# Performance work log

Hardware: AMD Instinct MI355X
Metric: run time of the kernel (lower is better)

## Reference

```python
import jax, jax.numpy as jnp
import numpy as np

# irreps as (multiplicity, l); parities match between in/hidden/out so every irrep has exactly one path
IRR_IN  = [(256, 0), (128, 1), (64, 2)]   # dim 256+384+320 = 960
IRR_H   = [(512, 0), (256, 1), (128, 2)]  # dim 512+768+640 = 1920
IRR_OUT = IRR_IN
N = 32768
EPS = 1e-8      # NormActivation epsilon
BN_EPS = 1e-5   # BatchNorm eps (e3nn default)


def _dim(irr):
    return sum(m * (2 * l + 1) for m, l in irr)


def _split(x, irr):
    """Split flat [N, dim] into per-irrep fields [N, mul, 2l+1]."""
    outs, o = [], 0
    for m, l in irr:
        d = m * (2 * l + 1)
        outs.append(x[:, o:o + d].reshape(x.shape[0], m, 2 * l + 1))
        o += d
    return outs


def _linear(x, w, irr_in, irr_out):
    """e3nn o3.Linear: per-irrep channel mixing with 1/sqrt(fan_in) path norm, no bias."""
    fields = _split(x, irr_in)
    outs, o = [], 0
    for f, (mi, l), (mo, _) in zip(fields, irr_in, irr_out):
        wk = w[o:o + mi * mo].reshape(mi, mo) * (1.0 / np.sqrt(mi))
        o += mi * mo
        outs.append(jnp.einsum('nui,uv->nvi', f, wk).reshape(f.shape[0], -1))
    return jnp.concatenate(outs, axis=1)


def _norm_act(x, irr):
    """e3nn NormActivation(scalar_nonlinearity=sigmoid, normalize=True): f * sigmoid(|f|)/|f|."""
    outs = []
    for f in _split(x, irr):
        n = jnp.sqrt(jnp.sum(f * f, axis=-1, keepdims=True) + EPS)
        outs.append((f * (jax.nn.sigmoid(n) / n)).reshape(f.shape[0], -1))
    return jnp.concatenate(outs, axis=1)


def _batch_norm(x, w, b, irr):
    """e3nn BatchNorm (training mode, reduce='mean', normalization='component').
    Scalars: standard batchnorm with weight+bias. l>0: divide by sqrt(batch-mean
    component-squared-norm), scale by weight."""
    outs, ow, ob = [], 0, 0
    for f, (m, l) in zip(_split(x, irr), irr):
        wk = w[ow:ow + m]; ow += m
        if l == 0:
            bk = b[ob:ob + m]; ob += m
            mu = jnp.mean(f, axis=0)                      # [m, 1]
            var = jnp.mean((f - mu) ** 2, axis=0)         # [m, 1]
            g = (f - mu) * (wk[:, None] / jnp.sqrt(var + BN_EPS)) + bk[:, None]
        else:
            n2 = jnp.mean(jnp.mean(f * f, axis=-1), axis=0)  # [m]
            g = f * (wk / jnp.sqrt(n2 + BN_EPS))[None, :, None]
        outs.append(g.reshape(f.shape[0], -1))
    return jnp.concatenate(outs, axis=1)


def setup_inputs() -> dict:
    key = jax.random.key(0)
    ks = jax.random.split(key, 5)
    n_w1 = sum(mi * mo for (mi, _), (mo, _) in zip(IRR_IN, IRR_H))    # 172032
    n_w2 = sum(mi * mo for (mi, _), (mo, _) in zip(IRR_H, IRR_H))     # 344064
    n_w3 = sum(mi * mo for (mi, _), (mo, _) in zip(IRR_H, IRR_OUT))   # 172032
    n_wb = sum(mi * mo for (mi, _), (mo, _) in zip(IRR_IN, IRR_OUT))  # 86016
    return {
        'x': jax.random.normal(ks[0], (N, _dim(IRR_IN)), dtype=jnp.float32),
        'w1': jax.random.normal(ks[1], (n_w1,), dtype=jnp.float32),
        'w2': jax.random.normal(ks[2], (n_w2,), dtype=jnp.float32),
        'w3': jax.random.normal(ks[3], (n_w3,), dtype=jnp.float32),
        'wb': jax.random.normal(ks[4], (n_wb,), dtype=jnp.float32),
        'bn_w': jnp.ones((448,), dtype=jnp.float32),
        'bn_b': jnp.zeros((256,), dtype=jnp.float32),
    }


def reference(x, w1, w2, w3, wb, bn_w, bn_b):
    out = _linear(x, w1, IRR_IN, IRR_H)
    out = _norm_act(out, IRR_H)
    out = _linear(out, w2, IRR_H, IRR_H)
    out = _norm_act(out, IRR_H)
    out = _linear(out, w3, IRR_H, IRR_OUT)
    out = _linear(x, wb, IRR_IN, IRR_OUT) + out
    return _batch_norm(out, bn_w, bn_b, IRR_OUT)
```

## Files before the change

### kernel.cpp

```cpp
#include <hip/hip_runtime.h>
#include <cstddef>
#include <cstdint>

#define DEVINL __device__ __forceinline__
typedef unsigned short u16;
typedef __attribute__((ext_vector_type(8))) short short8;
typedef __attribute__((ext_vector_type(4))) float f32x4;
#define MFMA16 __builtin_amdgcn_mfma_f32_16x16x32_bf16

constexpr int NROW = 32768;
constexpr int CM   = 8192;

constexpr size_t WT_B    = 0;
constexpr size_t STATS_B = 3014656;
constexpr size_t XS0_B   = 3017728;
constexpr size_t X1_B    = 53349376;
constexpr size_t X2_B    = 103681024;
constexpr size_t H1S0_B  = 145624064;
constexpr size_t H1S1_B  = 162401280;
constexpr size_t H1S2_B  = 187567104;
constexpr size_t Y0F_B   = 145624064;
constexpr size_t Y1_B    = 179178496;
constexpr size_t Y2_B    = 204344320;
constexpr size_t WS_NEED = 225315840;


DEVINL u16 f2bf(float f) { union { float f; unsigned u; } c; c.f = f;
    unsigned r = (c.u + 0x7fffu + ((c.u >> 16) & 1u)) >> 16; return (u16)r; }
DEVINL float bf2f(u16 b) { union { unsigned u; float f; } c; c.u = ((unsigned)b) << 16; return c.f; }
DEVINL short8 ld8(const u16* p) { return *(const short8*)p; }

DEVINL void gload16(const u16* g, u16* l) {
    __builtin_amdgcn_global_load_lds(
        (const __attribute__((address_space(1))) unsigned*)g,
        (__attribute__((address_space(3))) unsigned*)l, 16, 0, 0);
}

__global__ void k_prep(const float* __restrict__ w1, const float* __restrict__ w2,
                       const float* __restrict__ w3, const float* __restrict__ wb,
                       u16* __restrict__ WT, float* __restrict__ stats)
{
    int t = blockIdx.x * 256 + threadIdx.x;
    if (t < 1507328) {
        const float iA = 0.08838834764831845f;
        const float iB = 0.044194173824159216f;
        const int   beg[12]  = {0,393216,458752,475136,999424,1130496,1163264,1294336,1327104,1335296,1466368,1499136};
        const int   rowW[12] = {768,256,128,1024,512,256,512,256,128,512,256,128};
        const int   l2K[12]  = {8,7,6,9,8,7,9,8,7,8,7,6};
        const int   srco[12] = {0,131072,163840,0,262144,327680,0,131072,163840,0,65536,81920};
        const int   arr[12]  = {0,0,0,1,1,1,2,2,2,3,3,3};
        const int   ld[12]   = {512,256,128,512,256,128,256,128,64,256,128,64};
        const float scl[12]  = {0.0625f,iA,0.125f,iB,0.0625f,iA,iB,0.0625f,iA,0.0625f,iA,0.125f};
        int s = 0;
        #pragma unroll
        for (int i = 1; i < 12; ++i) s += (t >= beg[i]) ? 1 : 0;
        int e    = t - beg[s];
        int v    = e / rowW[s];
        int rem  = e - v * rowW[s];
        int limb = rem >> l2K[s];
        int u    = rem & ((1 << l2K[s]) - 1);
        const float* srcs[4] = {w1, w2, w3, wb};
        float val = srcs[arr[s]][srco[s] + u * ld[s] + v] * scl[s];
        u16 h = f2bf(val);  float r1 = val - bf2f(h);
        u16 m = f2bf(r1);   float r2 = r1 - bf2f(m);
        WT[t] = (limb == 0) ? h : (limb == 1) ? m : f2bf(r2);
    } else {
        int q = t - 1507328;
        if (q < 704) stats[q] = 0.f;
    }
}

__global__ void k_xconv(const float* __restrict__ x, u16* __restrict__ xs0,
                        u16* __restrict__ x1, u16* __restrict__ x2)
{
    int g = blockIdx.x * 256 + threadIdx.x;
    if (g < 1048576) {
        int n = g >> 5, u0 = (g & 31) * 8;
        const float* s = x + (size_t)n * 960 + u0;
        float4 f0 = *(const float4*)s;
        float4 f1 = *(const float4*)(s + 4);
        float f[8] = {f0.x,f0.y,f0.z,f0.w,f1.x,f1.y,f1.z,f1.w};
        short8 oh, om, ol;
        #pragma unroll
        for (int j = 0; j < 8; ++j) {
            u16 h = f2bf(f[j]); float r1 = f[j] - bf2f(h);
            u16 m = f2bf(r1);   float r2 = r1 - bf2f(m);
            oh[j] = (short)h; om[j] = (short)m; ol[j] = (short)f2bf(r2);
        }
        size_t d = (size_t)n * 768 + u0;
        *(short8*)(xs0 + d) = oh;
        *(short8*)(xs0 + d + 256) = om;
        *(short8*)(xs0 + d + 512) = ol;
        return;
    }
    float f[8]; u16* dst; int halfW;
    if (g < 2621440) {
        int gl = g - 1048576;
        int i = gl >> 19, r = gl & 524287;
        int n = r >> 4, u0 = (r & 15) * 8;
        const float* s = x + (size_t)n * 960 + 256 + (size_t)u0 * 3 + i;
        #pragma unroll
        for (int j = 0; j < 8; ++j) f[j] = s[j * 3];
        dst = x1 + (size_t)i * 8388608 + (size_t)n * 256 + u0;
        halfW = 128;
    } else {
        int gl = g - 2621440;
        int i = gl >> 18, r = gl & 262143;
        int n = r >> 3, u0 = (r & 7) * 8;
        const float* s = x + (size_t)n * 960 + 640 + (size_t)u0 * 5 + i;
        #pragma unroll
        for (int j = 0; j < 8; ++j) f[j] = s[j * 5];
        dst = x2 + (size_t)i * 4194304 + (size_t)n * 128 + u0;
        halfW = 64;
    }
    short8 oh, ol;
    #pragma unroll
    for (int j = 0; j < 8; ++j) {
        u16 h = f2bf(f[j]);
        oh[j] = (short)h;
        ol[j] = (short)f2bf(f[j] - bf2f(h));
    }
    *(short8*)dst = oh;
    *(short8*)(dst + halfW) = ol;
}

template<int NT, int EP, bool TS, bool SEG2>
__global__ __launch_bounds__(256) void k_gemm(
    const u16* __restrict__ A1, long A1ps, int A1cmb, int A1rs,
    int K1, int k1t, int T1, unsigned a1map, unsigned b1map,
    const u16* __restrict__ B1, int B1rs,
    const u16* __restrict__ A2, long A2ps, int A2cmb, int A2rs,
    int K2, int k2t, unsigned a2map, unsigned b2map,
    const u16* __restrict__ B2, int B2rs,
    int Stot, int tsTiles,
    u16* __restrict__ outB, float* __restrict__ outF,
    long Ops, int Ocmb, int Ors, int loOff, int cbs)
{
    constexpr int BN = NT * 32;
    __shared__ u16 lds[2][128 * 64];

    int b = blockIdx.x;
    int xcd = b & 7, jj = b >> 3;
    int rb = xcd + ((jj >> cbs) << 3);
    int cb = jj & ((1 << cbs) - 1);
    int rb128 = rb << 7;

    int tix = threadIdx.x, lane = tix & 63, w = tix >> 6;
    int wm64 = (w >> 1) << 6;
    int wn = w & 1;

    const u16* a1row = A1 + (size_t)(rb128 >> A1cmb) * A1ps
                          + (size_t)(rb128 & ((1 << A1cmb) - 1)) * A1rs;
    const u16* a2row = nullptr;
    if constexpr (SEG2)
        a2row = A2 + (size_t)(rb128 >> A2cmb) * A2ps
                   + (size_t)(rb128 & ((1 << A2cmb) - 1)) * A2rs;

    auto stage = [&](int t, int buf) {
        const u16* art; int rs, col0;
        if (!SEG2 || t < T1) {
            int sg = t >> k1t, off = (t & ((1 << k1t) - 1)) << 6;
            art = a1row; rs = A1rs;
            col0 = (int)((a1map >> (2 * sg)) & 3u) * K1 + off;
        } else {
            int tt = t - T1;
            int sg = tt >> k2t, off = (tt & ((1 << k2t) - 1)) << 6;
            art = a2row; rs = A2rs;
            col0 = (int)((a2map >> (2 * sg)) & 3u) * K2 + off;
        }
        #pragma unroll
        for (int i = 0; i < 4; ++i) {
            int seg = (w << 2) | i;
            int tr  = (seg << 3) + (lane >> 3);
            int sl  = lane & 7;
            const u16* src = art + (size_t)tr * rs + col0 + ((sl ^ (tr & 7)) << 3);
            gload16(src, &lds[buf][seg * 512]);
        }
    };

    f32x4 z = {0.f, 0.f, 0.f, 0.f};
    f32x4 acc[4][NT], S[4][NT], E[4][NT];
    #pragma unroll
    for (int mt = 0; mt < 4; ++mt)
        #pragma unroll
        for (int nt = 0; nt < NT; ++nt) { acc[mt][nt] = z; if constexpr (TS) { S[mt][nt] = z; E[mt][nt] = z; } }

    stage(0, 0);
    asm volatile("s_waitcnt vmcnt(0)" ::: "memory");
    __syncthreads();

    int colbase = cb * BN + wn * (NT * 16) + (lane & 15);
    int cur = 0;
    for (int s = 0; s < Stot; ++s) {
        const u16* bp; int brs, bcol;
        if (!SEG2 || s < T1) {
            int sg = s >> k1t;
            bcol = (int)((b1map >> (2 * sg)) & 3u) * K1 + ((s & ((1 << k1t) - 1)) << 6);
            bp = B1; brs = B1rs;
        } else {
            int tt = s - T1; int sg = tt >> k2t;
            bcol = (int)((b2map >> (2 * sg)) & 3u) * K2 + ((tt & ((1 << k2t) - 1)) << 6);
            bp = B2; brs = B2rs;
        }
        short8 breg[NT][2];
        #pragma unroll
        for (int nt = 0; nt < NT; ++nt)
            #pragma unroll
            for (int h = 0; h < 2; ++h)
                breg[nt][h] = ld8(bp + (size_t)(colbase + nt * 16) * brs + bcol + h * 32 + ((lane >> 4) << 3));

        if (s + 1 < Stot) stage(s + 1, cur ^ 1);

        bool tsT = TS && (s < tsTiles);
        #pragma unroll
        for (int h = 0; h < 2; ++h) {
            short8 a[4];
            #pragma unroll
            for (int mt = 0; mt < 4; ++mt) {
                int tr = wm64 + mt * 16 + (lane & 15);
                int slot = h * 4 + (lane >> 4);
                a[mt] = *(const short8*)&lds[cur][tr * 64 + ((slot ^ (tr & 7)) << 3)];
            }
            if (tsT) {
                #pragma unroll
                for (int mt = 0; mt < 4; ++mt)
                    #pragma unroll
                    for (int nt = 0; nt < NT; ++nt) {
                        f32x4 d = MFMA16(a[mt], breg[nt][h], z, 0, 0, 0);
                        #pragma unroll
                        for (int r = 0; r < 4; ++r) {
                            float aa = S[mt][nt][r], bb = d[r];
                            float sm = aa + bb;
                            float tt2 = sm - aa;
                            float er = (aa - (sm - tt2)) + (bb - tt2);
                            S[mt][nt][r] = sm;
                            E[mt][nt][r] += er;
                        }
                    }
            } else {
                #pragma unroll
                for (int mt = 0; mt < 4; ++mt)
                    #pragma unroll
                    for (int nt = 0; nt < NT; ++nt)
                        acc[mt][nt] = MFMA16(a[mt], breg[nt][h], acc[mt][nt], 0, 0, 0);
            }
        }
        asm volatile("s_waitcnt vmcnt(0)" ::: "memory");
        __syncthreads();
        cur ^= 1;
    }

    size_t obase = (size_t)(rb128 >> Ocmb) * Ops + (size_t)(rb128 & ((1 << Ocmb) - 1)) * Ors;
    #pragma unroll
    for (int mt = 0; mt < 4; ++mt) {
        #pragma unroll
        for (int r = 0; r < 4; ++r) {
            int lrow = wm64 + mt * 16 + ((lane >> 4) << 2) + r;
            size_t ro = obase + (size_t)lrow * Ors;
            #pragma unroll
            for (int nt = 0; nt < NT; ++nt) {
                int colg = cb * BN + wn * (NT * 16) + nt * 16 + (lane & 15);
                float p = acc[mt][nt][r];
                if constexpr (TS) p = S[mt][nt][r] + (E[mt][nt][r] + p);
                if constexpr (EP == 1) {
                    outF[ro + colg] = p;
                } else {
                    float v = p;
                    if constexpr (EP == 2 || EP == 3) {
                        float nrm = sqrtf(p * p + 1e-8f);
                        v = p / ((1.0f + expf(-nrm)) * nrm);
                    }
                    u16 hi = f2bf(v);
                    outB[ro + colg] = hi;
                    if constexpr (EP == 3 || EP == 4)
                        outB[ro + colg + loOff] = f2bf(v - bf2f(hi));
                }
            }
        }
    }
}

template<int C, bool SPL>
__global__ __launch_bounds__(256) void k_normact(u16* __restrict__ buf, long PS,
                                                 int l2g, int halfW, long total8)
{
    long idx = (long)blockIdx.x * 256 + threadIdx.x;
    if (idx >= total8) return;
    long r  = idx >> l2g;
    int  cg = (int)(idx & ((1 << l2g) - 1));
    int  W  = SPL ? (halfW << 1) : halfW;
    size_t off = (size_t)r * W + (size_t)cg * 8;
    float f[C][8];
    #pragma unroll
    for (int i = 0; i < C; ++i) {
        short8 h = ld8(buf + (size_t)i * PS + off);
        if constexpr (SPL) {
            short8 l = ld8(buf + (size_t)i * PS + off + halfW);
            #pragma unroll
            for (int j = 0; j < 8; ++j) f[i][j] = bf2f((u16)h[j]) + bf2f((u16)l[j]);
        } else {
            #pragma unroll
            for (int j = 0; j < 8; ++j) f[i][j] = bf2f((u16)h[j]);
        }
    }
    #pragma unroll
    for (int j = 0; j < 8; ++j) {
        float s2 = 1e-8f;
        #pragma unroll
        for (int i = 0; i < C; ++i) s2 += f[i][j] * f[i][j];
        float nrm = sqrtf(s2);
        float scl = 1.0f / ((1.0f + __expf(-nrm)) * nrm);
        #pragma unroll
        for (int i = 0; i < C; ++i) f[i][j] *= scl;
    }
    #pragma unroll
    for (int i = 0; i < C; ++i) {
        short8 oh, ol;
        #pragma unroll
        for (int j = 0; j < 8; ++j) {
            u16 hi = f2bf(f[i][j]);
            oh[j] = (short)hi;
            if constexpr (SPL) ol[j] = (short)f2bf(f[i][j] - bf2f(hi));
        }
        *(short8*)(buf + (size_t)i * PS + off) = oh;
        if constexpr (SPL) *(short8*)(buf + (size_t)i * PS + off + halfW) = ol;
    }
}

__global__ void k_stats(const float* __restrict__ y0f, const u16* __restrict__ y1,
                        const u16* __restrict__ y2, float* __restrict__ stats)
{
    int sec = blockIdx.y, t = threadIdx.x;
    int r0 = blockIdx.x * 512;
    float sm = 0.f, sq = 0.f;
    if (sec == 0) {
        int v = t;
        for (int r = r0; r < r0 + 512; ++r) {
            float val = y0f[(size_t)r * 256 + v];
            sm += val; sq += val * val;
        }
        atomicAdd(&stats[v], sm);
        atomicAdd(&stats[256 + v], sq);
    } else if (sec == 1) {
        int v = t & 127, sub = t >> 7;
        for (int r = r0 + sub; r < r0 + 512; r += 2)
            #pragma unroll
            for (int p = 0; p < 3; ++p) {
                float val = bf2f(y1[(size_t)p * 4194304 + (size_t)r * 128 + v]);
                sq += val * val;
            }
        __shared__ float S2[256];
        S2[t] = sq; __syncthreads();
        if (t < 128) atomicAdd(&stats[512 + v], sq + S2[t + 128]);
    } else {
        int v = t & 63, sub = t >> 6;
        for (int r = r0 + sub; r < r0 + 512; r += 4)
            #pragma unroll
            for (int p = 0; p < 5; ++p) {
                float val = bf2f(y2[(size_t)p * 2097152 + (size_t)r * 64 + v]);
                sq += val * val;
            }
        __shared__ float S2[256];
        S2[t] = sq; __syncthreads();
        if (t < 64) atomicAdd(&stats[640 + v], sq + S2[t + 64] + S2[t + 128] + S2[t + 192]);
    }
}

__global__ __launch_bounds__(448) void k_bnapply(
    const float* __restrict__ y0f, const u16* __restrict__ y1, const u16* __restrict__ y2,
    const float* __restrict__ stats, const float* __restrict__ bnw, const float* __restrict__ bnb,
    float* __restrict__ out)
{
    int n = blockIdx.x, t = threadIdx.x;
    const float invN = 1.f / 32768.f;
    if (t < 256) {
        float mu  = stats[t] * invN;
        float var = stats[256 + t] * invN - mu * mu;
        float a   = bnw[t] * rsqrtf(var + 1e-5f);
        out[(size_t)n * 960 + t] = (y0f[(size_t)n * 256 + t] - mu) * a + bnb[t];
    } else if (t < 384) {
        int v = t - 256;
        float a = bnw[256 + v] * rsqrtf(stats[512 + v] * (invN / 3.f) + 1e-5f);
        #pragma unroll
        for (int i = 0; i < 3; ++i)
            out[(size_t)n * 960 + 256 + v * 3 + i] =
                bf2f(y1[(size_t)i * 4194304 + (size_t)n * 128 + v]) * a;
    } else {
        int v = t - 384;
        float a = bnw[384 + v] * rsqrtf(stats[640 + v] * (invN / 5.f) + 1e-5f);
        #pragma unroll
        for (int i = 0; i < 5; ++i)
            out[(size_t)n * 960 + 640 + v * 5 + i] =
                bf2f(y2[(size_t)i * 2097152 + (size_t)n * 64 + v]) * a;
    }
}

extern "C" void kernel_launch(void* const* d_in, const int* in_sizes, int n_in,
                              void* d_out, int out_size, void* d_ws, size_t ws_size,
                              hipStream_t stream)
{
    const float* x   = (const float*)d_in[0];
    const float* w1  = (const float*)d_in[1];
    const float* w2  = (const float*)d_in[2];
    const float* w3  = (const float*)d_in[3];
    const float* wb  = (const float*)d_in[4];
    const float* bnw = (const float*)d_in[5];
    const float* bnb = (const float*)d_in[6];
    float* out = (float*)d_out;

    if (ws_size < WS_NEED) return;

    char* ws = (char*)d_ws;
    u16*   WT    = (u16*)(ws + WT_B);
    float* stats = (float*)(ws + STATS_B);
    u16*   xs0   = (u16*)(ws + XS0_B);
    u16*   x1    = (u16*)(ws + X1_B);
    u16*   x2    = (u16*)(ws + X2_B);
    u16*   h1s0  = (u16*)(ws + H1S0_B);
    u16*   h1s1  = (u16*)(ws + H1S1_B);
    u16*   h1s2  = (u16*)(ws + H1S2_B);
    float* y0f   = (float*)(ws + Y0F_B);
    u16*   y1    = (u16*)(ws + Y1_B);
    u16*   y2    = (u16*)(ws + Y2_B);
    u16*   h2s0  = (u16*)d_out;
    u16*   h2s1  = h2s0 + 16777216;
    u16*   h2s2  = h2s0 + 41943040;

    k_prep <<<5891, 256, 0, stream>>>(w1, w2, w3, wb, WT, stats);
    k_xconv<<<15360, 256, 0, stream>>>(x, xs0, x1, x2);

    for (int c = 0; c < NROW / CM; ++c) {
        size_t r0 = (size_t)c * CM;
        k_gemm<2, 3, true, false><<<512, 256, 0, stream>>>(
            xs0 + r0 * 768, 0L, 30, 768,
            256, 2, 24, 580u, 2128u, WT + 0, 768,
            nullptr, 0L, 30, 64, 64, 0, 0u, 0u, nullptr, 64,
            24, 4,
            h1s0, nullptr, 0L, 30, 1024, 512, 3);
        k_gemm<4, 4, false, false><<<384, 256, 0, stream>>>(
            x1 + r0 * 256, 8388608L, 13, 256,
            128, 1, 6, 4u, 16u, WT + 393216, 256,
            nullptr, 0L, 30, 64, 64, 0, 0u, 0u, nullptr, 64,
            6, 0,
            h1s1, nullptr, 4194304L, 13, 512, 256, 1);
        k_gemm<4, 4, false, false><<<320, 256, 0, stream>>>(
            x2 + r0 * 128, 4194304L, 13, 128,
            64, 0, 3, 4u, 16u, WT + 458752, 128,
            nullptr, 0L, 30, 64, 64, 0, 0u, 0u, nullptr, 64,
            3, 0,
            h1s2, nullptr, 2097152L, 13, 256, 128, 0);
        k_normact<3, true><<<1024, 256, 0, stream>>>(h1s1, 4194304L, 5, 256, 262144L);
        k_normact<5, true><<<512,  256, 0, stream>>>(h1s2, 2097152L, 4, 128, 131072L);
        k_gemm<4, 2, false, false><<<256, 256, 0, stream>>>(
            h1s0, 0L, 30, 1024,
            512, 3, 24, 4u, 16u, WT + 475136, 1024,
            nullptr, 0L, 30, 64, 64, 0, 0u, 0u, nullptr, 64,
            24, 0,
            h2s0 + r0 * 512, nullptr, 0L, 30, 512, 0, 2);
        k_gemm<4, 0, false, false><<<384, 256, 0, stream>>>(
            h1s1, 4194304L, 13, 512,
            256, 2, 12, 4u, 16u, WT + 999424, 512,
            nullptr, 0L, 30, 64, 64, 0, 0u, 0u, nullptr, 64,
            12, 0,
            h2s1 + r0 * 256, nullptr, 8388608L, 13, 256, 0, 1);
        k_gemm<4, 0, false, false><<<320, 256, 0, stream>>>(
            h1s2, 2097152L, 13, 256,
            128, 1, 6, 4u, 16u, WT + 1130496, 256,
            nullptr, 0L, 30, 64, 64, 0, 0u, 0u, nullptr, 64,
            6, 0,
            h2s2 + r0 * 128, nullptr, 4194304L, 13, 128, 0, 0);
    }
    k_normact<3, false><<<4096, 256, 0, stream>>>(h2s1, 8388608L, 5, 256, 1048576L);
    k_normact<5, false><<<2048, 256, 0, stream>>>(h2s2, 4194304L, 4, 128, 524288L);

    k_gemm<4, 1, false, true><<<512, 256, 0, stream>>>(
        h2s0, 0L, 30, 512,
        512, 3, 8, 0u, 0u, WT + 1163264, 512,
        xs0, 0L, 30, 768,
        256, 2, 4u, 16u, WT + 1335296, 512,
        20, 0,
        nullptr, y0f, 0L, 30, 256, 0, 1);
    k_gemm<4, 0, false, true><<<768, 256, 0, stream>>>(
        h2s1, 8388608L, 15, 256,
        256, 2, 4, 0u, 0u, WT + 1294336, 256,
        x1, 8388608L, 15, 256,
        128, 1, 4u, 16u, WT + 1466368, 256,
        10, 0,
        y1, nullptr, 4194304L, 15, 128, 0, 0);
    k_gemm<2, 0, false, true><<<1280, 256, 0, stream>>>(
        h2s2, 4194304L, 15, 128,
        128, 1, 2, 0u, 0u, WT + 1327104, 128,
        x2, 4194304L, 15, 128,
        64, 0, 4u, 16u, WT + 1499136, 128,
        5, 0,
        y2, nullptr, 2097152L, 15, 64, 0, 0);

    k_stats  <<<dim3(64, 3), 256, 0, stream>>>(y0f, y1, y2, stats);
    k_bnapply<<<32768, 448, 0, stream>>>(y0f, y1, y2, stats, bnw, bnb, out);
}
```

Baseline: 1.363 ms.

## Merge per-irrep GEMMs into grouped launches with triple-buffered LDS pipeline

Groups the three per-irrep GEMMs of each layer into one launch that dispatches on block index through a descriptor struct. It also fuses the two norm-activation kernels and rewrites input conversion to stage rows in LDS for coalesced reads. The GEMM main loop moves from double to triple buffering with partial vmcnt waits, so two tiles are in flight and barriers are lighter. Block-to-tile mapping drops the XCD-aware swizzle, and stats uses more blocks. The aim is fewer launches, less tail idle time and better load/compute overlap, at the cost of extra LDS per block (lower occupancy) and possibly worse L2 locality.

```diff
diff --git a/kernel.cpp b/kernel.cpp
--- a/kernel.cpp
+++ b/kernel.cpp
@@ -23,7 +23,6 @@
 constexpr size_t Y1_B    = 179178496;
 constexpr size_t Y2_B    = 204344320;
 constexpr size_t WS_NEED = 225315840;
-
 
 DEVINL u16 f2bf(float f) { union { float f; unsigned u; } c; c.f = f;
     unsigned r = (c.u + 0x7fffu + ((c.u >> 16) & 1u)) >> 16; return (u16)r; }
@@ -70,111 +69,109 @@
     }
 }
 
-__global__ void k_xconv(const float* __restrict__ x, u16* __restrict__ xs0,
-                        u16* __restrict__ x1, u16* __restrict__ x2)
-{
-    int g = blockIdx.x * 256 + threadIdx.x;
-    if (g < 1048576) {
-        int n = g >> 5, u0 = (g & 31) * 8;
-        const float* s = x + (size_t)n * 960 + u0;
-        float4 f0 = *(const float4*)s;
-        float4 f1 = *(const float4*)(s + 4);
-        float f[8] = {f0.x,f0.y,f0.z,f0.w,f1.x,f1.y,f1.z,f1.w};
-        short8 oh, om, ol;
+__global__ __launch_bounds__(256) void k_xconv(const float* __restrict__ x,
+    u16* __restrict__ xs0, u16* __restrict__ x1, u16* __restrict__ x2)
+{
+    __shared__ float xl[15360];
+    int t = threadIdx.x;
+    int n0 = blockIdx.x * 16;
+    const float* src = x + (size_t)n0 * 960;
+    #pragma unroll
+    for (int i = 0; i < 15; ++i) {
+        float4 v = *(const float4*)(src + (size_t)(i * 256 + t) * 4);
+        *(float4*)&xl[(i * 256 + t) * 4] = v;
+    }
+    __syncthreads();
+    #pragma unroll
+    for (int k = 0; k < 17; ++k) {
+        int id = k * 256 + t;
+        float f[8]; u16* dst; int limb;
+        if (id < 1536) {
+            limb = id >> 9; int rem = id & 511;
+            int r = rem >> 5, g = rem & 31;
+            #pragma unroll
+            for (int j = 0; j < 8; ++j) f[j] = xl[r * 960 + g * 8 + j];
+            dst = xs0 + (size_t)(n0 + r) * 768 + limb * 256 + g * 8;
+        } else if (id < 3072) {
+            int id1 = id - 1536;
+            limb = id1 / 768; int rem = id1 % 768;
+            int i = rem >> 8; int rem2 = rem & 255;
+            int r = rem2 >> 4, g = rem2 & 15;
+            #pragma unroll
+            for (int j = 0; j < 8; ++j) f[j] = xl[r * 960 + 256 + (g * 8 + j) * 3 + i];
+            dst = x1 + (size_t)i * 8388608 + (size_t)(n0 + r) * 256 + limb * 128 + g * 8;
+        } else {
+            int id2 = id - 3072;
+            limb = id2 / 640; int rem = id2 % 640;
+            int i = rem >> 7; int rem2 = rem & 127;
+            int r = rem2 >> 3, g = rem2 & 7;
+            #pragma unroll
+            for (int j = 0; j < 8; ++j) f[j] = xl[r * 960 + 640 + (g * 8 + j) * 5 + i];
+            dst = x2 + (size_t)i * 4194304 + (size_t)(n0 + r) * 128 + limb * 64 + g * 8;
+        }
+        short8 o;
         #pragma unroll
         for (int j = 0; j < 8; ++j) {
-            u16 h = f2bf(f[j]); float r1 = f[j] - bf2f(h);
-            u16 m = f2bf(r1);   float r2 = r1 - bf2f(m);
-            oh[j] = (short)h; om[j] = (short)m; ol[j] = (short)f2bf(r2);
-        }
-        size_t d = (size_t)n * 768 + u0;
-        *(short8*)(xs0 + d) = oh;
-        *(short8*)(xs0 + d + 256) = om;
-        *(short8*)(xs0 + d + 512) = ol;
-        return;
-    }
-    float f[8]; u16* dst; int halfW;
-    if (g < 2621440) {
-        int gl = g - 1048576;
-        int i = gl >> 19, r = gl & 524287;
-        int n = r >> 4, u0 = (r & 15) * 8;
-        const float* s = x + (size_t)n * 960 + 256 + (size_t)u0 * 3 + i;
-        #pragma unroll
-        for (int j = 0; j < 8; ++j) f[j] = s[j * 3];
-        dst = x1 + (size_t)i * 8388608 + (size_t)n * 256 + u0;
-        halfW = 128;
-    } else {
-        int gl = g - 2621440;
-        int i = gl >> 18, r = gl & 262143;
-        int n = r >> 3, u0 = (r & 7) * 8;
-        const float* s = x + (size_t)n * 960 + 640 + (size_t)u0 * 5 + i;
-        #pragma unroll
-        for (int j = 0; j < 8; ++j) f[j] = s[j * 5];
-        dst = x2 + (size_t)i * 4194304 + (size_t)n * 128 + u0;
-        halfW = 64;
-    }
-    short8 oh, ol;
-    #pragma unroll
-    for (int j = 0; j < 8; ++j) {
-        u16 h = f2bf(f[j]);
-        oh[j] = (short)h;
-        ol[j] = (short)f2bf(f[j] - bf2f(h));
-    }
-    *(short8*)dst = oh;
-    *(short8*)(dst + halfW) = ol;
-}
+            float v = f[j];
+            u16 h = f2bf(v);
+            if (limb == 0) { o[j] = (short)h; }
+            else {
+                float r1 = v - bf2f(h);
+                u16 m = f2bf(r1);
+                o[j] = (limb == 1) ? (short)m : (short)f2bf(r1 - bf2f(m));
+            }
+        }
+        *(short8*)dst = o;
+    }
+}
+
+struct SecDesc {
+    const u16* A1; const u16* A2; const u16* B1; const u16* B2;
+    u16* outB; float* outF;
+    long A1ps, A2ps, Ops;
+    unsigned a1map, b1map, a2map, b2map;
+    int A1cmb, A1rs, K1, k1t, T1, B1rs;
+    int A2cmb, A2rs, K2, k2t, B2rs;
+    int Stot, tsTiles, Ocmb, Ors, loOff, nrb, bid0;
+};
+struct Sec3 { SecDesc d[3]; };
 
 template<int NT, int EP, bool TS, bool SEG2>
-__global__ __launch_bounds__(256) void k_gemm(
-    const u16* __restrict__ A1, long A1ps, int A1cmb, int A1rs,
-    int K1, int k1t, int T1, unsigned a1map, unsigned b1map,
-    const u16* __restrict__ B1, int B1rs,
-    const u16* __restrict__ A2, long A2ps, int A2cmb, int A2rs,
-    int K2, int k2t, unsigned a2map, unsigned b2map,
-    const u16* __restrict__ B2, int B2rs,
-    int Stot, int tsTiles,
-    u16* __restrict__ outB, float* __restrict__ outF,
-    long Ops, int Ocmb, int Ors, int loOff, int cbs)
+DEVINL void gemm_body(u16* lds, const SecDesc& d, int bid)
 {
     constexpr int BN = NT * 32;
-    __shared__ u16 lds[2][128 * 64];
-
-    int b = blockIdx.x;
-    int xcd = b & 7, jj = b >> 3;
-    int rb = xcd + ((jj >> cbs) << 3);
-    int cb = jj & ((1 << cbs) - 1);
+    int idx = bid - d.bid0;
+    int rb = idx % d.nrb, cb = idx / d.nrb;
     int rb128 = rb << 7;
-
     int tix = threadIdx.x, lane = tix & 63, w = tix >> 6;
-    int wm64 = (w >> 1) << 6;
-    int wn = w & 1;
-
-    const u16* a1row = A1 + (size_t)(rb128 >> A1cmb) * A1ps
-                          + (size_t)(rb128 & ((1 << A1cmb) - 1)) * A1rs;
+    int wm64 = (w >> 1) << 6, wn = w & 1;
+
+    const u16* a1row = d.A1 + (size_t)(rb128 >> d.A1cmb) * d.A1ps
+                            + (size_t)(rb128 & ((1 << d.A1cmb) - 1)) * (size_t)d.A1rs;
     const u16* a2row = nullptr;
     if constexpr (SEG2)
-        a2row = A2 + (size_t)(rb128 >> A2cmb) * A2ps
-                   + (size_t)(rb128 & ((1 << A2cmb) - 1)) * A2rs;
+        a2row = d.A2 + (size_t)(rb128 >> d.A2cmb) * d.A2ps
+                     + (size_t)(rb128 & ((1 << d.A2cmb) - 1)) * (size_t)d.A2rs;
 
     auto stage = [&](int t, int buf) {
         const u16* art; int rs, col0;
-        if (!SEG2 || t < T1) {
-            int sg = t >> k1t, off = (t & ((1 << k1t) - 1)) << 6;
-            art = a1row; rs = A1rs;
-            col0 = (int)((a1map >> (2 * sg)) & 3u) * K1 + off;
+        if (!SEG2 || t < d.T1) {
+            int sg = t >> d.k1t, off = (t & ((1 << d.k1t) - 1)) << 6;
+            art = a1row; rs = d.A1rs;
+            col0 = (int)((d.a1map >> (2 * sg)) & 3u) * d.K1 + off;
         } else {
-            int tt = t - T1;
-            int sg = tt >> k2t, off = (tt & ((1 << k2t) - 1)) << 6;
-            art = a2row; rs = A2rs;
-            col0 = (int)((a2map >> (2 * sg)) & 3u) * K2 + off;
+            int tt = t - d.T1;
+            int sg = tt >> d.k2t, off = (tt & ((1 << d.k2t) - 1)) << 6;
+            art = a2row; rs = d.A2rs;
+            col0 = (int)((d.a2map >> (2 * sg)) & 3u) * d.K2 + off;
         }
         #pragma unroll
         for (int i = 0; i < 4; ++i) {
             int seg = (w << 2) | i;
             int tr  = (seg << 3) + (lane >> 3);
             int sl  = lane & 7;
-            const u16* src = art + (size_t)tr * rs + col0 + ((sl ^ (tr & 7)) << 3);
-            gload16(src, &lds[buf][seg * 512]);
+            gload16(art + (size_t)tr * rs + col0 + ((sl ^ (tr & 7)) << 3),
+                    lds + buf * 8192 + seg * 512);
         }
     };
 
@@ -186,21 +183,19 @@
         for (int nt = 0; nt < NT; ++nt) { acc[mt][nt] = z; if constexpr (TS) { S[mt][nt] = z; E[mt][nt] = z; } }
 
     stage(0, 0);
-    asm volatile("s_waitcnt vmcnt(0)" ::: "memory");
-    __syncthreads();
-
+    stage(1, 1);
     int colbase = cb * BN + wn * (NT * 16) + (lane & 15);
     int cur = 0;
-    for (int s = 0; s < Stot; ++s) {
+    for (int s = 0; s < d.Stot; ++s) {
         const u16* bp; int brs, bcol;
-        if (!SEG2 || s < T1) {
-            int sg = s >> k1t;
-            bcol = (int)((b1map >> (2 * sg)) & 3u) * K1 + ((s & ((1 << k1t) - 1)) << 6);
-            bp = B1; brs = B1rs;
+        if (!SEG2 || s < d.T1) {
+            int sg = s >> d.k1t;
+            bcol = (int)((d.b1map >> (2 * sg)) & 3u) * d.K1 + ((s & ((1 << d.k1t) - 1)) << 6);
+            bp = d.B1; brs = d.B1rs;
         } else {
-            int tt = s - T1; int sg = tt >> k2t;
-            bcol = (int)((b2map >> (2 * sg)) & 3u) * K2 + ((tt & ((1 << k2t) - 1)) << 6);
-            bp = B2; brs = B2rs;
+            int tt = s - d.T1, sg = tt >> d.k2t;
+            bcol = (int)((d.b2map >> (2 * sg)) & 3u) * d.K2 + ((tt & ((1 << d.k2t) - 1)) << 6);
+            bp = d.B2; brs = d.B2rs;
         }
         short8 breg[NT][2];
         #pragma unroll
@@ -209,9 +204,17 @@
             for (int h = 0; h < 2; ++h)
                 breg[nt][h] = ld8(bp + (size_t)(colbase + nt * 16) * brs + bcol + h * 32 + ((lane >> 4) << 3));
 
-        if (s + 1 < Stot) stage(s + 1, cur ^ 1);
-
-        bool tsT = TS && (s < tsTiles);
+        int nb = cur + 2; if (nb >= 3) nb -= 3;
+        if (s + 2 < d.Stot) {
+            stage(s + 2, nb);
+            asm volatile("s_waitcnt vmcnt(8)" ::: "memory");
+        } else {
+            asm volatile("s_waitcnt vmcnt(0)" ::: "memory");
+        }
+        asm volatile("s_barrier" ::: "memory");
+
+        const u16* lbuf = lds + cur * 8192;
+        bool tsT = TS && (s < d.tsTiles);
         #pragma unroll
         for (int h = 0; h < 2; ++h) {
             short8 a[4];
@@ -219,17 +222,17 @@
             for (int mt = 0; mt < 4; ++mt) {
                 int tr = wm64 + mt * 16 + (lane & 15);
                 int slot = h * 4 + (lane >> 4);
-                a[mt] = *(const short8*)&lds[cur][tr * 64 + ((slot ^ (tr & 7)) << 3)];
+                a[mt] = *(const short8*)&lbuf[tr * 64 + ((slot ^ (tr & 7)) << 3)];
             }
             if (tsT) {
                 #pragma unroll
                 for (int mt = 0; mt < 4; ++mt)
                     #pragma unroll
                     for (int nt = 0; nt < NT; ++nt) {
-                        f32x4 d = MFMA16(a[mt], breg[nt][h], z, 0, 0, 0);
+                        f32x4 dd = MFMA16(a[mt], breg[nt][h], z, 0, 0, 0);
                         #pragma unroll
                         for (int r = 0; r < 4; ++r) {
-                            float aa = S[mt][nt][r], bb = d[r];
+                            float aa = S[mt][nt][r], bb = dd[r];
                             float sm = aa + bb;
                             float tt2 = sm - aa;
                             float er = (aa - (sm - tt2)) + (bb - tt2);
@@ -245,25 +248,24 @@
                         acc[mt][nt] = MFMA16(a[mt], breg[nt][h], acc[mt][nt], 0, 0, 0);
             }
         }
-        asm volatile("s_waitcnt vmcnt(0)" ::: "memory");
-        __syncthreads();
-        cur ^= 1;
-    }
-
-    size_t obase = (size_t)(rb128 >> Ocmb) * Ops + (size_t)(rb128 & ((1 << Ocmb) - 1)) * Ors;
+        asm volatile("s_barrier" ::: "memory");
+        cur = (cur + 1 == 3) ? 0 : cur + 1;
+    }
+
+    size_t obase = (size_t)(rb128 >> d.Ocmb) * d.Ops + (size_t)(rb128 & ((1 << d.Ocmb) - 1)) * (size_t)d.Ors;
     #pragma unroll
     for (int mt = 0; mt < 4; ++mt) {
         #pragma unroll
         for (int r = 0; r < 4; ++r) {
             int lrow = wm64 + mt * 16 + ((lane >> 4) << 2) + r;
-            size_t ro = obase + (size_t)lrow * Ors;
+            size_t ro = obase + (size_t)lrow * d.Ors;
             #pragma unroll
             for (int nt = 0; nt < NT; ++nt) {
                 int colg = cb * BN + wn * (NT * 16) + nt * 16 + (lane & 15);
                 float p = acc[mt][nt][r];
                 if constexpr (TS) p = S[mt][nt][r] + (E[mt][nt][r] + p);
                 if constexpr (EP == 1) {
-                    outF[ro + colg] = p;
+                    d.outF[ro + colg] = p;
                 } else {
                     float v = p;
                     if constexpr (EP == 2 || EP == 3) {
@@ -271,20 +273,44 @@
                         v = p / ((1.0f + expf(-nrm)) * nrm);
                     }
                     u16 hi = f2bf(v);
-                    outB[ro + colg] = hi;
+                    d.outB[ro + colg] = hi;
                     if constexpr (EP == 3 || EP == 4)
-                        outB[ro + colg + loOff] = f2bf(v - bf2f(hi));
+                        d.outB[ro + colg + d.loOff] = f2bf(v - bf2f(hi));
                 }
             }
         }
     }
 }
 
+__global__ __launch_bounds__(256) void k_L1(Sec3 ds)
+{
+    __shared__ u16 lds[24576];
+    int bid = blockIdx.x;
+    if (bid < ds.d[1].bid0)      gemm_body<2, 3, true,  false>(lds, ds.d[0], bid);
+    else if (bid < ds.d[2].bid0) gemm_body<4, 4, false, false>(lds, ds.d[1], bid);
+    else                         gemm_body<4, 4, false, false>(lds, ds.d[2], bid);
+}
+__global__ __launch_bounds__(256) void k_L2(Sec3 ds)
+{
+    __shared__ u16 lds[24576];
+    int bid = blockIdx.x;
+    if (bid < ds.d[1].bid0)      gemm_body<4, 2, false, false>(lds, ds.d[0], bid);
+    else if (bid < ds.d[2].bid0) gemm_body<4, 0, false, false>(lds, ds.d[1], bid);
+    else                         gemm_body<4, 0, false, false>(lds, ds.d[2], bid);
+}
+__global__ __launch_bounds__(256) void k_L3(Sec3 ds)
+{
+    __shared__ u16 lds[24576];
+    int bid = blockIdx.x;
+    if (bid < ds.d[1].bid0)      gemm_body<4, 1, false, true>(lds, ds.d[0], bid);
+    else if (bid < ds.d[2].bid0) gemm_body<4, 0, false, true>(lds, ds.d[1], bid);
+    else                         gemm_body<2, 0, false, true>(lds, ds.d[2], bid);
+}
+
 template<int C, bool SPL>
-__global__ __launch_bounds__(256) void k_normact(u16* __restrict__ buf, long PS,
-                                                 int l2g, int halfW, long total8)
-{
-    long idx = (long)blockIdx.x * 256 + threadIdx.x;
+DEVINL void na_body(u16* __restrict__ buf, long PS, int l2g, int halfW, long total8, long bb)
+{
+    long idx = bb * 256 + threadIdx.x;
     if (idx >= total8) return;
     long r  = idx >> l2g;
     int  cg = (int)(idx & ((1 << l2g) - 1));
@@ -327,15 +353,25 @@
     }
 }
 
+template<bool SPL>
+__global__ __launch_bounds__(256) void k_na(
+    u16* b3, long PS3, int l2g3, int hw3, long t83,
+    u16* b5, long PS5, int l2g5, int hw5, long t85, int blk5)
+{
+    int bid = blockIdx.x;
+    if (bid < blk5) na_body<3, SPL>(b3, PS3, l2g3, hw3, t83, bid);
+    else            na_body<5, SPL>(b5, PS5, l2g5, hw5, t85, bid - blk5);
+}
+
 __global__ void k_stats(const float* __restrict__ y0f, const u16* __restrict__ y1,
                         const u16* __restrict__ y2, float* __restrict__ stats)
 {
     int sec = blockIdx.y, t = threadIdx.x;
-    int r0 = blockIdx.x * 512;
+    int r0 = blockIdx.x * 256;
     float sm = 0.f, sq = 0.f;
     if (sec == 0) {
         int v = t;
-        for (int r = r0; r < r0 + 512; ++r) {
+        for (int r = r0; r < r0 + 256; ++r) {
             float val = y0f[(size_t)r * 256 + v];
             sm += val; sq += val * val;
         }
@@ -343,7 +379,7 @@
         atomicAdd(&stats[256 + v], sq);
     } else if (sec == 1) {
         int v = t & 127, sub = t >> 7;
-        for (int r = r0 + sub; r < r0 + 512; r += 2)
+        for (int r = r0 + sub; r < r0 + 256; r += 2)
             #pragma unroll
             for (int p = 0; p < 3; ++p) {
                 float val = bf2f(y1[(size_t)p * 4194304 + (size_t)r * 128 + v]);
@@ -354,7 +390,7 @@
         if (t < 128) atomicAdd(&stats[512 + v], sq + S2[t + 128]);
     } else {
         int v = t & 63, sub = t >> 6;
-        for (int r = r0 + sub; r < r0 + 512; r += 4)
+        for (int r = r0 + sub; r < r0 + 256; r += 4)
             #pragma unroll
             for (int p = 0; p < 5; ++p) {
                 float val = bf2f(y2[(size_t)p * 2097152 + (size_t)r * 64 + v]);
@@ -393,6 +429,29 @@
             out[(size_t)n * 960 + 640 + v * 5 + i] =
                 bf2f(y2[(size_t)i * 2097152 + (size_t)n * 64 + v]) * a;
     }
+}
+
+static SecDesc mk(const u16* A1, long A1ps, int A1cmb, int A1rs,
+                  int K1, int k1t, int T1, unsigned a1map, unsigned b1map,
+                  const u16* B1, int B1rs,
+                  const u16* A2, long A2ps, int A2cmb, int A2rs,
+                  int K2, int k2t, unsigned a2map, unsigned b2map,
+                  const u16* B2, int B2rs,
+                  int Stot, int tsTiles,
+                  u16* outB, float* outF, long Ops, int Ocmb, int Ors, int loOff,
+                  int nrb, int bid0)
+{
+    SecDesc d;
+    d.A1 = A1; d.A1ps = A1ps; d.A1cmb = A1cmb; d.A1rs = A1rs;
+    d.K1 = K1; d.k1t = k1t; d.T1 = T1; d.a1map = a1map; d.b1map = b1map;
+    d.B1 = B1; d.B1rs = B1rs;
+    d.A2 = A2; d.A2ps = A2ps; d.A2cmb = A2cmb; d.A2rs = A2rs;
+    d.K2 = K2; d.k2t = k2t; d.a2map = a2map; d.b2map = b2map;
+    d.B2 = B2; d.B2rs = B2rs;
+    d.Stot = Stot; d.tsTiles = tsTiles;
+    d.outB = outB; d.outF = outF; d.Ops = Ops; d.Ocmb = Ocmb; d.Ors = Ors; d.loOff = loOff;
+    d.nrb = nrb; d.bid0 = bid0;
+    return d;
 }
 
 extern "C" void kernel_launch(void* const* d_in, const int* in_sizes, int n_in,
@@ -427,74 +486,53 @@
     u16*   h2s2  = h2s0 + 41943040;
 
     k_prep <<<5891, 256, 0, stream>>>(w1, w2, w3, wb, WT, stats);
-    k_xconv<<<15360, 256, 0, stream>>>(x, xs0, x1, x2);
+    k_xconv<<<2048, 256, 0, stream>>>(x, xs0, x1, x2);
 
     for (int c = 0; c < NROW / CM; ++c) {
         size_t r0 = (size_t)c * CM;
-        k_gemm<2, 3, true, false><<<512, 256, 0, stream>>>(
-            xs0 + r0 * 768, 0L, 30, 768,
-            256, 2, 24, 580u, 2128u, WT + 0, 768,
-            nullptr, 0L, 30, 64, 64, 0, 0u, 0u, nullptr, 64,
-            24, 4,
-            h1s0, nullptr, 0L, 30, 1024, 512, 3);
-        k_gemm<4, 4, false, false><<<384, 256, 0, stream>>>(
-            x1 + r0 * 256, 8388608L, 13, 256,
-            128, 1, 6, 4u, 16u, WT + 393216, 256,
-            nullptr, 0L, 30, 64, 64, 0, 0u, 0u, nullptr, 64,
-            6, 0,
-            h1s1, nullptr, 4194304L, 13, 512, 256, 1);
-        k_gemm<4, 4, false, false><<<320, 256, 0, stream>>>(
-            x2 + r0 * 128, 4194304L, 13, 128,
-            64, 0, 3, 4u, 16u, WT + 458752, 128,
-            nullptr, 0L, 30, 64, 64, 0, 0u, 0u, nullptr, 64,
-            3, 0,
-            h1s2, nullptr, 2097152L, 13, 256, 128, 0);
-        k_normact<3, true><<<1024, 256, 0, stream>>>(h1s1, 4194304L, 5, 256, 262144L);
-        k_normact<5, true><<<512,  256, 0, stream>>>(h1s2, 2097152L, 4, 128, 131072L);
-        k_gemm<4, 2, false, false><<<256, 256, 0, stream>>>(
-            h1s0, 0L, 30, 1024,
-            512, 3, 24, 4u, 16u, WT + 475136, 1024,
-            nullptr, 0L, 30, 64, 64, 0, 0u, 0u, nullptr, 64,
-            24, 0,
-            h2s0 + r0 * 512, nullptr, 0L, 30, 512, 0, 2);
-        k_gemm<4, 0, false, false><<<384, 256, 0, stream>>>(
-            h1s1, 4194304L, 13, 512,
-            256, 2, 12, 4u, 16u, WT + 999424, 512,
-            nullptr, 0L, 30, 64, 64, 0, 0u, 0u, nullptr, 64,
-            12, 0,
-            h2s1 + r0 * 256, nullptr, 8388608L, 13, 256, 0, 1);
-        k_gemm<4, 0, false, false><<<320, 256, 0, stream>>>(
-            h1s2, 2097152L, 13, 256,
-            128, 1, 6, 4u, 16u, WT + 1130496, 256,
-            nullptr, 0L, 30, 64, 64, 0, 0u, 0u, nullptr, 64,
-            6, 0,
-            h2s2 + r0 * 128, nullptr, 4194304L, 13, 128, 0, 0);
-    }
-    k_normact<3, false><<<4096, 256, 0, stream>>>(h2s1, 8388608L, 5, 256, 1048576L);
-    k_normact<5, false><<<2048, 256, 0, stream>>>(h2s2, 4194304L, 4, 128, 524288L);
-
-    k_gemm<4, 1, false, true><<<512, 256, 0, stream>>>(
-        h2s0, 0L, 30, 512,
-        512, 3, 8, 0u, 0u, WT + 1163264, 512,
-        xs0, 0L, 30, 768,
-        256, 2, 4u, 16u, WT + 1335296, 512,
-        20, 0,
-        nullptr, y0f, 0L, 30, 256, 0, 1);
-    k_gemm<4, 0, false, true><<<768, 256, 0, stream>>>(
-        h2s1, 8388608L, 15, 256,
-        256, 2, 4, 0u, 0u, WT + 1294336, 256,
-        x1, 8388608L, 15, 256,
-        128, 1, 4u, 16u, WT + 1466368, 256,
-        10, 0,
-        y1, nullptr, 4194304L, 15, 128, 0, 0);
-    k_gemm<2, 0, false, true><<<1280, 256, 0, stream>>>(
-        h2s2, 4194304L, 15, 128,
-        128, 1, 2, 0u, 0u, WT + 1327104, 128,
-        x2, 4194304L, 15, 128,
-        64, 0, 4u, 16u, WT + 1499136, 128,
-        5, 0,
-        y2, nullptr, 2097152L, 15, 64, 0, 0);
-
-    k_stats  <<<dim3(64, 3), 256, 0, stream>>>(y0f, y1, y2, stats);
+        Sec3 dl1;
+        dl1.d[0] = mk(xs0 + r0 * 768, 0L, 30, 768, 256, 2, 24, 580u, 2128u, WT + 0, 768,
+                      nullptr, 0L, 30, 64, 64, 0, 0u, 0u, nullptr, 64,
+                      24, 4, h1s0, nullptr, 0L, 30, 1024, 512, 64, 0);
+        dl1.d[1] = mk(x1 + r0 * 256, 8388608L, 13, 256, 128, 1, 6, 4u, 16u, WT + 393216, 256,
+                      nullptr, 0L, 30, 64, 64, 0, 0u, 0u, nullptr, 64,
+                      6, 0, h1s1, nullptr, 4194304L, 13, 512, 256, 192, 512);
+        dl1.d[2] = mk(x2 + r0 * 128, 4194304L, 13, 128, 64, 0, 3, 4u, 16u, WT + 458752, 128,
+                      nullptr, 0L, 30, 64, 64, 0, 0u, 0u, nullptr, 64,
+                      3, 0, h1s2, nullptr, 2097152L, 13, 256, 128, 320, 896);
+        k_L1<<<1216, 256, 0, stream>>>(dl1);
+
+        k_na<true><<<1536, 256, 0, stream>>>(h1s1, 4194304L, 5, 256, 262144L,
+                                             h1s2, 2097152L, 4, 128, 131072L, 1024);
+
+        Sec3 dl2;
+        dl2.d[0] = mk(h1s0, 0L, 30, 1024, 512, 3, 24, 4u, 16u, WT + 475136, 1024,
+                      nullptr, 0L, 30, 64, 64, 0, 0u, 0u, nullptr, 64,
+                      24, 0, h2s0 + r0 * 512, nullptr, 0L, 30, 512, 0, 64, 0);
+        dl2.d[1] = mk(h1s1, 4194304L, 13, 512, 256, 2, 12, 4u, 16u, WT + 999424, 512,
+                      nullptr, 0L, 30, 64, 64, 0, 0u, 0u, nullptr, 64,
+                      12, 0, h2s1 + r0 * 256, nullptr, 8388608L, 13, 256, 0, 192, 256);
+        dl2.d[2] = mk(h1s2, 2097152L, 13, 256, 128, 1, 6, 4u, 16u, WT + 1130496, 256,
+                      nullptr, 0L, 30, 64, 64, 0, 0u, 0u, nullptr, 64,
+                      6, 0, h2s2 + r0 * 128, nullptr, 4194304L, 13, 128, 0, 320, 640);
+        k_L2<<<960, 256, 0, stream>>>(dl2);
+    }
+
+    k_na<false><<<6144, 256, 0, stream>>>(h2s1, 8388608L, 5, 256, 1048576L,
+                                          h2s2, 4194304L, 4, 128, 524288L, 4096);
+
+    Sec3 dl3;
+    dl3.d[0] = mk(h2s0, 0L, 30, 512, 512, 3, 8, 0u, 0u, WT + 1163264, 512,
+                  xs0, 0L, 30, 768, 256, 2, 4u, 16u, WT + 1335296, 512,
+                  20, 0, nullptr, y0f, 0L, 30, 256, 0, 256, 0);
+    dl3.d[1] = mk(h2s1, 8388608L, 15, 256, 256, 2, 4, 0u, 0u, WT + 1294336, 256,
+                  x1, 8388608L, 15, 256, 128, 1, 4u, 16u, WT + 1466368, 256,
+                  10, 0, y1, nullptr, 4194304L, 15, 128, 0, 768, 512);
+    dl3.d[2] = mk(h2s2, 4194304L, 15, 128, 128, 1, 2, 0u, 0u, WT + 1327104, 128,
+                  x2, 4194304L, 15, 128, 64, 0, 4u, 16u, WT + 1499136, 128,
+                  5, 0, y2, nullptr, 2097152L, 15, 64, 0, 1280, 1280);
+    k_L3<<<2560, 256, 0, stream>>>(dl3);
+
+    k_stats  <<<dim3(128, 3), 256, 0, stream>>>(y0f, y1, y2, stats);
     k_bnapply<<<32768, 448, 0, stream>>>(y0f, y1, y2, stats, bnw, bnb, out);
 }
```

Measured after the change: 1.098 ms. 19.5% less time.
